# Performance work log

Hardware: AMD Instinct MI355X
Metric: run time of the kernel (lower is better)

The kernel has to match this reference:

```python
import jax, jax.numpy as jnp
import numpy as np

NV, NU, FT, HID, OUT, NE = 50000, 50000, 128, 256, 128, 800000


def _seg_sum(x, seg, n):
    return jax.ops.segment_sum(x, seg, num_segments=n)


def _seg_mean(x, seg, n):
    s = _seg_sum(x, seg, n)
    cnt = _seg_sum(jnp.ones((x.shape[0], 1), x.dtype), seg, n)
    return s / jnp.maximum(cnt, 1.0)


def _prelu(x, a):
    return jnp.where(x >= 0, x, a * x)


def setup_inputs() -> dict:
    key = jax.random.key(0)
    ks = jax.random.split(key, 12)
    lin = lambda k, i, o: jax.random.normal(k, (i, o), jnp.float32) * (1.0 / np.sqrt(i))
    slope = jnp.full((1,), 0.25, jnp.float32)  # nn.PReLU() default
    return {
        'features_v': jax.random.normal(ks[0], (NV, FT), jnp.float32),
        'features_u': jax.random.normal(ks[1], (NU, FT), jnp.float32),
        'edge_v': jax.random.randint(ks[2], (NE,), 0, NV, jnp.int32),
        'edge_u': jax.random.randint(ks[3], (NE,), 0, NU, jnp.int32),
        'Wv1': lin(ks[4], FT, HID), 'bv1': jnp.zeros((HID,), jnp.float32), 'av1': slope,
        'Wu1': lin(ks[5], FT, HID), 'bu1': jnp.zeros((HID,), jnp.float32), 'au1': slope,
        'Wv2': lin(ks[6], HID, OUT), 'bv2': jnp.zeros((OUT,), jnp.float32), 'av2': slope,
        'Wu2': lin(ks[7], HID, OUT), 'bu2': jnp.zeros((OUT,), jnp.float32), 'au2': slope,
        'Wv3': lin(ks[8], OUT + FT, OUT), 'bv3': jnp.zeros((OUT,), jnp.float32),
        'Wu3': lin(ks[9], OUT + FT, OUT), 'bu3': jnp.zeros((OUT,), jnp.float32),
    }


def reference(features_v, features_u, edge_v, edge_u,
              Wv1, bv1, av1, Wu1, bu1, au1,
              Wv2, bv2, av2, Wu2, bu2, au2,
              Wv3, bv3, Wu3, bu3):
    # stage 1: mean of raw neighbor features across the bipartite relation
    vneighbor = _seg_mean(features_u[edge_u], edge_v, NV)   # [NV, FT]
    uneighbor = _seg_mean(features_v[edge_v], edge_u, NU)   # [NU, FT]
    ve1 = _prelu(vneighbor @ Wv1 + bv1, av1)                # [NV, HID]
    ue1 = _prelu(uneighbor @ Wu1 + bu1, au1)                # [NU, HID]
    # stage 2: mean of transformed neighbor embeddings
    ve2 = _prelu(_seg_mean(ue1[edge_u], edge_v, NV) @ Wv2 + bv2, av2)  # [NV, OUT]
    ue2 = _prelu(_seg_mean(ve1[edge_v], edge_u, NU) @ Wu2 + bu2, au2)  # [NU, OUT]
    # stage 3: concat with raw features, Identity activation
    ve3 = jnp.concatenate([ve2, features_v], 1) @ Wv3 + bv3  # [NV, OUT]
    ue3 = jnp.concatenate([ue2, features_u], 1) @ Wu3 + bu3  # [NU, OUT]
    # self-inclusive neighbor mean: mean over {neighbors' emb, own emb}
    deg_v = _seg_sum(jnp.ones((NE, 1), ve3.dtype), edge_v, NV)
    deg_u = _seg_sum(jnp.ones((NE, 1), ue3.dtype), edge_u, NU)
    sv = (_seg_sum(ue3[edge_u], edge_v, NV) + ve3) / (deg_v + 1.0)  # [NV, OUT]
    su = (_seg_sum(ve3[edge_v], edge_u, NU) + ue3) / (deg_u + 1.0)  # [NU, OUT]
    # node_embs = mean over the single relation = (ve2, ue2); pack all outputs
    out_v = jnp.concatenate([ve2, sv], 1)  # [NV, 2*OUT]
    out_u = jnp.concatenate([ue2, su], 1)  # [NU, 2*OUT]
    return jnp.stack([out_v, out_u])       # [2, N, 2*OUT]
```

## Files before the change

### kernel.cpp

```cpp
#include <hip/hip_runtime.h>
#include <stdint.h>

#define NVN 50000
#define NUN 50000
#define NB 49
#define CH 4096
#define HCH 8192
#define BCAP 24576

typedef __attribute__((ext_vector_type(8))) short short8v;
typedef __attribute__((ext_vector_type(8))) unsigned short ushort8v;
typedef __attribute__((ext_vector_type(4))) float float4v;

__device__ __forceinline__ unsigned short f2bf(float f) {
  union { float f; unsigned u; } x; x.f = f;
  unsigned r = x.u + 0x7FFFu + ((x.u >> 16) & 1u);
  return (unsigned short)(r >> 16);
}
__device__ __forceinline__ float bf2f(unsigned short h) {
  union { unsigned u; float f; } x; x.u = ((unsigned)h) << 16;
  return x.f;
}

struct WConvEnt { const float* src; unsigned short* dst; int K; int N; };
struct PrepArgs {
  WConvEnt w[6];
  const float* fv; const float* fu;
  unsigned short* fbv; unsigned short* fbu;
  const int* ev; const int* eu;
  int* bcnt;
  int ne;
};
__global__ __launch_bounds__(256) void prep_kernel(PrepArgs a) {
  __shared__ int h[2 * NB];
  int b = blockIdx.x;
  if (b < 768) {
    WConvEnt c = a.w[b >> 7];
    int i = (b & 127) * 256 + threadIdx.x;
    int k = i / c.N, n = i - k * c.N;
    c.dst[(size_t)n * c.K + k] = f2bf(c.src[i]);
    return;
  }
  b -= 768;
  if (b < 6250) {
    const float* src = (b < 3125) ? a.fv : a.fu;
    unsigned short* dst = (b < 3125) ? a.fbv : a.fbu;
    int bb = (b < 3125) ? b : b - 3125;
    size_t base = ((size_t)bb * 256 + threadIdx.x) * 8;
    float4 x = *(const float4*)(src + base);
    float4 y = *(const float4*)(src + base + 4);
    ushort8v r;
    r[0] = f2bf(x.x); r[1] = f2bf(x.y); r[2] = f2bf(x.z); r[3] = f2bf(x.w);
    r[4] = f2bf(y.x); r[5] = f2bf(y.y); r[6] = f2bf(y.z); r[7] = f2bf(y.w);
    *(ushort8v*)(dst + base) = r;
    return;
  }
  b -= 6250;
  const int tid = threadIdx.x;
  for (int j = tid; j < 2 * NB; j += 256) h[j] = 0;
  __syncthreads();
  const int e0 = b * HCH;
  const int e1 = min(e0 + HCH, a.ne);
  for (int i = e0 + tid; i < e1; i += 256) {
    atomicAdd(&h[a.ev[i] >> 10], 1);
    atomicAdd(&h[NB + (a.eu[i] >> 10)], 1);
  }
  __syncthreads();
  for (int j = tid; j < 2 * NB; j += 256)
    if (h[j]) atomicAdd(&a.bcnt[j], h[j]);
}

__global__ __launch_bounds__(64) void tiny_scan(const int* __restrict__ bcnt,
                                                int* __restrict__ bbase,
                                                int* __restrict__ bcur) {
  if (threadIdx.x == 0) {
    int acc = 0;
    for (int b = 0; b < NB; ++b) { bbase[b] = acc; bcur[b] = acc; acc += bcnt[b]; }
    bbase[NB] = acc;
    acc = 0;
    for (int b = 0; b < NB; ++b) {
      bbase[NB + 1 + b] = acc; bcur[NB + b] = acc; acc += bcnt[NB + b];
    }
    bbase[2 * NB + 1] = acc;
  }
}

__global__ __launch_bounds__(256) void bucket_scatter(
    const int* __restrict__ ev, const int* __restrict__ eu,
    int* __restrict__ bcur_v, int* __restrict__ bcur_u,
    unsigned* __restrict__ stg_v, unsigned* __restrict__ stg_u, int ne) {
  __shared__ int cnt[NB];
  __shared__ int pos[NB];
  __shared__ int gbase[NB];
  __shared__ unsigned rec[CH];
  const int side = blockIdx.y;
  const int* key = side ? eu : ev;
  const int* pay = side ? ev : eu;
  int* bcur = side ? bcur_u : bcur_v;
  unsigned* stg = side ? stg_u : stg_v;
  const int tid = threadIdx.x;
  const int e0 = blockIdx.x * CH;
  const int e1 = min(e0 + CH, ne);
  if (tid < NB) cnt[tid] = 0;
  __syncthreads();
  for (int i = e0 + tid; i < e1; i += 256) atomicAdd(&cnt[key[i] >> 10], 1);
  __syncthreads();
  if (tid < 64) {
    int c = (tid < NB) ? cnt[tid] : 0;
    int x = c;
#pragma unroll
    for (int s = 1; s < 64; s <<= 1) {
      int t = __shfl_up(x, (unsigned)s, 64);
      if (tid >= s) x += t;
    }
    if (tid < NB) pos[tid] = x - c;
  }
  __syncthreads();
  for (int i = e0 + tid; i < e1; i += 256) {
    int k = key[i];
    int b = k >> 10;
    int p = atomicAdd(&pos[b], 1);
    rec[p] = ((unsigned)(k & 1023) << 16) | (unsigned)pay[i];
  }
  __syncthreads();
  if (tid < NB) gbase[tid] = atomicAdd(&bcur[tid], cnt[tid]);
  __syncthreads();
  for (int b = 0; b < NB; ++b) {
    int c = cnt[b];
    int lbase = pos[b] - c;
    int gb = gbase[b];
    for (int i = tid; i < c; i += 256) stg[gb + i] = rec[lbase + i];
  }
}

__global__ __launch_bounds__(256) void bucket_build(
    int* __restrict__ off_v, int* __restrict__ off_u,
    const int* __restrict__ bbase,
    const unsigned* __restrict__ stg_v, const unsigned* __restrict__ stg_u,
    unsigned short* __restrict__ csr_v, unsigned short* __restrict__ csr_u,
    int nv, int nu) {
  __shared__ int cur[1024];
  __shared__ int wred[4];
  __shared__ int wbase[4];
  __shared__ unsigned short st[BCAP];
  const int side = blockIdx.y;
  int* off = side ? off_u : off_v;
  const unsigned* stg = side ? stg_u : stg_v;
  unsigned short* csr = side ? csr_u : csr_v;
  const int n = side ? nu : nv;
  const int* bb = bbase + side * (NB + 1);
  const int nbase = blockIdx.x << 10;
  const int nb = min(1024, n - nbase);
  const int ebase = bb[blockIdx.x];
  const int cnt = bb[blockIdx.x + 1] - ebase;
  const int tid = threadIdx.x;
  const int lane = tid & 63;
  const int w = tid >> 6;

  for (int j = tid; j < 1024; j += 256) cur[j] = 0;
  __syncthreads();
  for (int i = tid; i < cnt; i += 256) atomicAdd(&cur[stg[ebase + i] >> 16], 1);
  __syncthreads();
  const int j0 = tid * 4;
  int c0 = cur[j0], c1 = cur[j0 + 1], c2 = cur[j0 + 2], c3 = cur[j0 + 3];
  int tsum = c0 + c1 + c2 + c3;
  int x = tsum;
#pragma unroll
  for (int s = 1; s < 64; s <<= 1) {
    int t = __shfl_up(x, (unsigned)s, 64);
    if (lane >= s) x += t;
  }
  if (lane == 63) wred[w] = x;
  __syncthreads();
  if (tid == 0) {
    int a = 0;
    for (int k = 0; k < 4; ++k) { wbase[k] = a; a += wred[k]; }
  }
  __syncthreads();
  const int ex = wbase[w] + (x - tsum);
  cur[j0] = ex;
  cur[j0 + 1] = ex + c0;
  cur[j0 + 2] = ex + c0 + c1;
  cur[j0 + 3] = ex + c0 + c1 + c2;
  __syncthreads();
  for (int j = tid; j < nb; j += 256) off[nbase + j] = ebase + cur[j];
  if (nbase + nb == n && tid == 0) off[n] = ebase + cnt;
  __syncthreads();
  if (cnt <= BCAP) {
    for (int i = tid; i < cnt; i += 256) {
      unsigned r = stg[ebase + i];
      int p = atomicAdd(&cur[r >> 16], 1);
      st[p] = (unsigned short)(r & 0xFFFFu);
    }
    __syncthreads();
    for (int i = tid; i < cnt; i += 256) csr[ebase + i] = st[i];
  } else {
    for (int i = tid; i < cnt; i += 256) {
      unsigned r = stg[ebase + i];
      int p = atomicAdd(&cur[r >> 16], 1);
      csr[ebase + p] = (unsigned short)(r & 0xFFFFu);
    }
  }
}

struct GSide {
  const unsigned* src;
  const unsigned short* csr; const int* off;
  const float* bias; const float* slope;
  const unsigned* own;
  void* dst; int ldo;
};

__device__ __forceinline__ void acc8(float* acc, uint4 p) {
  acc[0] += bf2f((unsigned short)p.x);
  acc[1] += bf2f((unsigned short)(p.x >> 16));
  acc[2] += bf2f((unsigned short)p.y);
  acc[3] += bf2f((unsigned short)(p.y >> 16));
  acc[4] += bf2f((unsigned short)p.z);
  acc[5] += bf2f((unsigned short)(p.z >> 16));
  acc[6] += bf2f((unsigned short)p.w);
  acc[7] += bf2f((unsigned short)(p.w >> 16));
}

template <int MODE>
__global__ __launch_bounds__(256) void gatherk(GSide g0, GSide g1, int n) {
  GSide g = blockIdx.y ? g1 : g0;
  int wid = (int)(((size_t)blockIdx.x * 256 + threadIdx.x) >> 6);
  if (wid >= n) return;
  const int lane = threadIdx.x & 63;
  const int grp = lane >> 4;
  const int lc = lane & 15;
  const int s = g.off[wid], e = g.off[wid + 1];
  const int cnt = e - s;
  float acc[8] = {0.f, 0.f, 0.f, 0.f, 0.f, 0.f, 0.f, 0.f};
  int idx = 0;
  if (lane < cnt) idx = (int)g.csr[s + lane];
  const int m = cnt < 64 ? cnt : 64;
  int j = 0;
  for (; j + 7 < m; j += 8) {
    int r0 = __shfl(idx, j + grp, 64);
    int r1 = __shfl(idx, j + 4 + grp, 64);
    uint4 p0 = *((const uint4*)(g.src + (size_t)r0 * 64) + lc);
    uint4 p1 = *((const uint4*)(g.src + (size_t)r1 * 64) + lc);
    acc8(acc, p0);
    acc8(acc, p1);
  }
  for (; j + 3 < m; j += 4) {
    int r0 = __shfl(idx, j + grp, 64);
    uint4 p0 = *((const uint4*)(g.src + (size_t)r0 * 64) + lc);
    acc8(acc, p0);
  }
  if (j < m) {
    int jj = j + grp;
    int r0 = __shfl(idx, jj < m ? jj : 0, 64);
    if (jj < m) {
      uint4 p0 = *((const uint4*)(g.src + (size_t)r0 * 64) + lc);
      acc8(acc, p0);
    }
  }
  for (int i = s + 64 + grp; i < e; i += 4) {
    int r0 = (int)g.csr[i];
    uint4 p0 = *((const uint4*)(g.src + (size_t)r0 * 64) + lc);
    acc8(acc, p0);
  }
#pragma unroll
  for (int k = 0; k < 8; ++k) {
    acc[k] += __shfl_xor(acc[k], 16, 64);
    acc[k] += __shfl_xor(acc[k], 32, 64);
  }
  if (grp != 0) return;
  const float deg = (float)cnt;
  if (MODE == 0) {
    float inv = 1.f / fmaxf(deg, 1.f);
    uint4 o;
    o.x = ((unsigned)f2bf(acc[1] * inv) << 16) | (unsigned)f2bf(acc[0] * inv);
    o.y = ((unsigned)f2bf(acc[3] * inv) << 16) | (unsigned)f2bf(acc[2] * inv);
    o.z = ((unsigned)f2bf(acc[5] * inv) << 16) | (unsigned)f2bf(acc[4] * inv);
    o.w = ((unsigned)f2bf(acc[7] * inv) << 16) | (unsigned)f2bf(acc[6] * inv);
    *((uint4*)((unsigned*)g.dst + (size_t)wid * g.ldo) + lc) = o;
  } else if (MODE == 1) {
    float inv = 1.f / fmaxf(deg, 1.f);
    float sl = g.slope[0];
    float4 b0 = *(const float4*)(g.bias + lc * 8);
    float4 b1 = *(const float4*)(g.bias + lc * 8 + 4);
    float o[8];
    o[0] = acc[0] * inv + b0.x; o[1] = acc[1] * inv + b0.y;
    o[2] = acc[2] * inv + b0.z; o[3] = acc[3] * inv + b0.w;
    o[4] = acc[4] * inv + b1.x; o[5] = acc[5] * inv + b1.y;
    o[6] = acc[6] * inv + b1.z; o[7] = acc[7] * inv + b1.w;
#pragma unroll
    for (int k = 0; k < 8; ++k) o[k] = o[k] >= 0.f ? o[k] : o[k] * sl;
    float* dp = (float*)g.dst + (size_t)wid * g.ldo + lc * 8;
    *(float4*)dp = make_float4(o[0], o[1], o[2], o[3]);
    *(float4*)(dp + 4) = make_float4(o[4], o[5], o[6], o[7]);
  } else {
    float inv = 1.f / (deg + 1.f);
    uint4 ow = *((const uint4*)(g.own + (size_t)wid * 64) + lc);
    float o[8];
    o[0] = (acc[0] + bf2f((unsigned short)ow.x)) * inv;
    o[1] = (acc[1] + bf2f((unsigned short)(ow.x >> 16))) * inv;
    o[2] = (acc[2] + bf2f((unsigned short)ow.y)) * inv;
    o[3] = (acc[3] + bf2f((unsigned short)(ow.y >> 16))) * inv;
    o[4] = (acc[4] + bf2f((unsigned short)ow.z)) * inv;
    o[5] = (acc[5] + bf2f((unsigned short)(ow.z >> 16))) * inv;
    o[6] = (acc[6] + bf2f((unsigned short)ow.w)) * inv;
    o[7] = (acc[7] + bf2f((unsigned short)(ow.w >> 16))) * inv;
    float* dp = (float*)g.dst + (size_t)wid * g.ldo + lc * 8;
    *(float4*)dp = make_float4(o[0], o[1], o[2], o[3]);
    *(float4*)(dp + 4) = make_float4(o[4], o[5], o[6], o[7]);
  }
}

struct GmSide {
  const void* A1; const void* A2;
  const unsigned short* Wt;
  const float* bias; const float* slope;
  void* C;
};

template <int BF>
__device__ __forceinline__ short8v load_a8(const void* A, size_t off) {
  if (BF) {
    return *(const short8v*)((const unsigned short*)A + off);
  } else {
    const float* p = (const float*)A + off;
    float4 x = *(const float4*)p;
    float4 y = *(const float4*)(p + 4);
    short8v r;
    r[0] = (short)f2bf(x.x); r[1] = (short)f2bf(x.y);
    r[2] = (short)f2bf(x.z); r[3] = (short)f2bf(x.w);
    r[4] = (short)f2bf(y.x); r[5] = (short)f2bf(y.y);
    r[6] = (short)f2bf(y.z); r[7] = (short)f2bf(y.w);
    return r;
  }
}

#define TILES 5

template <int KB1, int KB2, int NF, int A1BF, int A2BF, int CBF, int ACT>
__global__ __launch_bounds__(256) void gemm_reg(GmSide s0, GmSide s1,
                                                int lda1, int lda2,
                                                int ldc, int M) {
  constexpr int KB = KB1 + KB2;
  GmSide s = blockIdx.z ? s1 : s0;
  const int K = KB * 32;
  const int tid = threadIdx.x;
  const int wv = tid >> 6;
  const int lane = tid & 63;
  const int lc = lane & 15;
  const int khi = lane >> 4;
  const int bm = blockIdx.x * (16 * TILES);
  const int colbase = wv * (NF * 16);

  short8v b[KB][NF];
#pragma unroll
  for (int kb = 0; kb < KB; ++kb)
#pragma unroll
    for (int f = 0; f < NF; ++f)
      b[kb][f] = *(const short8v*)(s.Wt + (size_t)(colbase + f * 16 + lc) * K +
                                   kb * 32 + khi * 8);

  const float sl = ACT ? s.slope[0] : 0.f;
  float bias_f[NF];
#pragma unroll
  for (int f = 0; f < NF; ++f)
    bias_f[f] = s.bias ? s.bias[colbase + f * 16 + lc] : 0.f;

  short8v a_cur[KB], a_nxt[KB];
  {
    const int rowa = bm + lc;
#pragma unroll
    for (int kb = 0; kb < KB; ++kb) {
      if (kb < KB1)
        a_cur[kb] = load_a8<A1BF>(s.A1, (size_t)rowa * lda1 + kb * 32 + khi * 8);
      else
        a_cur[kb] = load_a8<A2BF>(s.A2, (size_t)rowa * lda2 + (kb - KB1) * 32 + khi * 8);
    }
  }

  for (int t = 0; t < TILES; ++t) {
    if (t + 1 < TILES) {
      const int rowa = bm + (t + 1) * 16 + lc;
#pragma unroll
      for (int kb = 0; kb < KB; ++kb) {
        if (kb < KB1)
          a_nxt[kb] = load_a8<A1BF>(s.A1, (size_t)rowa * lda1 + kb * 32 + khi * 8);
        else
          a_nxt[kb] = load_a8<A2BF>(s.A2, (size_t)rowa * lda2 + (kb - KB1) * 32 + khi * 8);
      }
    }
    float4v acc[NF];
#pragma unroll
    for (int f = 0; f < NF; ++f) acc[f] = (float4v){0.f, 0.f, 0.f, 0.f};
#pragma unroll
    for (int kb = 0; kb < KB; ++kb)
#pragma unroll
      for (int f = 0; f < NF; ++f)
        acc[f] = __builtin_amdgcn_mfma_f32_16x16x32_bf16(a_cur[kb], b[kb][f],
                                                         acc[f], 0, 0, 0);
#pragma unroll
    for (int f = 0; f < NF; ++f) {
      const int col = colbase + f * 16 + lc;
#pragma unroll
      for (int i = 0; i < 4; ++i) {
        const int row = bm + t * 16 + khi * 4 + i;
        float v = acc[f][i] + bias_f[f];
        if (ACT && v < 0.f) v *= sl;
        if (CBF) ((unsigned short*)s.C)[(size_t)row * ldc + col] = f2bf(v);
        else     ((float*)s.C)[(size_t)row * ldc + col] = v;
      }
    }
#pragma unroll
    for (int kb = 0; kb < KB; ++kb) a_cur[kb] = a_nxt[kb];
  }
}

extern "C" void kernel_launch(void* const* d_in, const int* in_sizes, int n_in,
                              void* d_out, int out_size, void* d_ws, size_t ws_size,
                              hipStream_t stream) {
  const float* features_v = (const float*)d_in[0];
  const float* features_u = (const float*)d_in[1];
  const int* edge_v = (const int*)d_in[2];
  const int* edge_u = (const int*)d_in[3];
  const float* Wv1 = (const float*)d_in[4];
  const float* bv1 = (const float*)d_in[5];
  const float* av1 = (const float*)d_in[6];
  const float* Wu1 = (const float*)d_in[7];
  const float* bu1 = (const float*)d_in[8];
  const float* au1 = (const float*)d_in[9];
  const float* Wv2 = (const float*)d_in[10];
  const float* bv2 = (const float*)d_in[11];
  const float* av2 = (const float*)d_in[12];
  const float* Wu2 = (const float*)d_in[13];
  const float* bu2 = (const float*)d_in[14];
  const float* au2 = (const float*)d_in[15];
  const float* Wv3 = (const float*)d_in[16];
  const float* bv3 = (const float*)d_in[17];
  const float* Wu3 = (const float*)d_in[18];
  const float* bu3 = (const float*)d_in[19];
  const int ne = in_sizes[2];

  int* bcnt = (int*)d_ws;
  int* bbase = bcnt + 2 * NB;
  int* bcur = bbase + 2 * (NB + 1);
  int* off_v = bcur + 2 * NB;
  int* off_u = off_v + NVN + 1;
  unsigned short* csr_v = (unsigned short*)(off_u + NUN + 1);
  unsigned short* csr_u = csr_v + ne;
  uintptr_t sbase = (((uintptr_t)(csr_u + ne)) + 15) & ~(uintptr_t)15;
  unsigned* stg_v = (unsigned*)sbase;
  unsigned* stg_u = stg_v + ne;
  unsigned short* P1b = (unsigned short*)(stg_u + ne);
  unsigned short* P2b = P1b + (size_t)NVN * 128;
  unsigned short* E1v = P2b + (size_t)NUN * 128;
  unsigned short* E1u = E1v + (size_t)NVN * 256;
  unsigned short* Wb = E1u + (size_t)NUN * 256;
  unsigned short* Fbv = Wb + 6 * 32768;
  unsigned short* Fbu = Fbv + (size_t)NVN * 128;
  unsigned short* Ve3b = E1v;
  unsigned short* Ue3b = E1u;

  float* out_v = (float*)d_out;
  float* out_u = out_v + (size_t)NVN * 256;

  const int hb = (ne + HCH - 1) / HCH;
  const dim3 gg((NVN * 64) / 256, 2);
  const dim3 gr(NVN / (16 * TILES), 1, 2);
  const dim3 gsc((ne + CH - 1) / CH, 2);
  const dim3 gbd(NB, 2);

  hipMemsetAsync(bcnt, 0, (size_t)(2 * NB) * 4, stream);
  PrepArgs pa;
  pa.w[0] = {Wv1, Wb + 0 * 32768, 128, 256};
  pa.w[1] = {Wu1, Wb + 1 * 32768, 128, 256};
  pa.w[2] = {Wv2, Wb + 2 * 32768, 256, 128};
  pa.w[3] = {Wu2, Wb + 3 * 32768, 256, 128};
  pa.w[4] = {Wv3, Wb + 4 * 32768, 256, 128};
  pa.w[5] = {Wu3, Wb + 5 * 32768, 256, 128};
  pa.fv = features_v; pa.fu = features_u;
  pa.fbv = Fbv; pa.fbu = Fbu;
  pa.ev = edge_v; pa.eu = edge_u;
  pa.bcnt = bcnt; pa.ne = ne;
  prep_kernel<<<768 + 6250 + hb, 256, 0, stream>>>(pa);
  tiny_scan<<<1, 64, 0, stream>>>(bcnt, bbase, bcur);
  bucket_scatter<<<gsc, 256, 0, stream>>>(edge_v, edge_u, bcur, bcur + NB,
                                          stg_v, stg_u, ne);
  bucket_build<<<gbd, 256, 0, stream>>>(off_v, off_u, bbase, stg_v, stg_u,
                                        csr_v, csr_u, NVN, NUN);

  {
    GSide a{(const unsigned*)Fbu, csr_v, off_v, nullptr, nullptr, nullptr, P1b, 64};
    GSide b{(const unsigned*)Fbv, csr_u, off_u, nullptr, nullptr, nullptr, P2b, 64};
    gatherk<0><<<gg, 256, 0, stream>>>(a, b, NVN);
  }
  {
    GmSide a{P1b, nullptr, Wb + 0 * 32768, bv1, av1, E1v};
    GmSide b{P2b, nullptr, Wb + 1 * 32768, bu1, au1, E1u};
    gemm_reg<4, 0, 4, 1, 0, 1, 1><<<gr, 256, 0, stream>>>(a, b, 128, 0, 256, NVN);
  }
  {
    GmSide a{E1v, nullptr, Wb + 3 * 32768, nullptr, nullptr, P1b};
    GmSide b{E1u, nullptr, Wb + 2 * 32768, nullptr, nullptr, P2b};
    gemm_reg<8, 0, 2, 1, 0, 1, 0><<<gr, 256, 0, stream>>>(a, b, 256, 0, 128, NVN);
  }
  {
    GSide a{(const unsigned*)P2b, csr_v, off_v, bv2, av2, nullptr, out_v, 256};
    GSide b{(const unsigned*)P1b, csr_u, off_u, bu2, au2, nullptr, out_u, 256};
    gatherk<1><<<gg, 256, 0, stream>>>(a, b, NVN);
  }
  {
    GmSide a{out_v, Fbv, Wb + 4 * 32768, bv3, nullptr, Ve3b};
    GmSide b{out_u, Fbu, Wb + 5 * 32768, bu3, nullptr, Ue3b};
    gemm_reg<4, 4, 2, 0, 1, 1, 0><<<gr, 256, 0, stream>>>(a, b, 256, 128, 128, NVN);
  }
  {
    GSide a{(const unsigned*)Ue3b, csr_v, off_v, nullptr, nullptr,
            (const unsigned*)Ve3b, out_v + 128, 256};
    GSide b{(const unsigned*)Ve3b, csr_u, off_u, nullptr, nullptr,
            (const unsigned*)Ue3b, out_u + 128, 256};
    gatherk<2><<<gg, 256, 0, stream>>>(a, b, NVN);
  }
}
```

Measured before the change: 422.8 us.

## Fuse layer-1 and layer-2 GEMMs via LDS and fold bucket scan into consumers

Replaces the two back-to-back GEMMs (P→E1 with bias+PReLU, then E1→P·W2) with a single kernel that keeps the 64x256 E1 tile in shared memory, so the 256-wide bf16 intermediate is never written to or re-read from global memory. The tiny single-thread scan kernel is removed: bucket_scatter and bucket_build each recompute the 49-bucket prefix sum with a wave shuffle, and bcur becomes a relative cursor zeroed by memset. This saves a launch and a large intermediate round trip. In exchange the fused kernel holds many register fragments and a 33KB LDS tile, which may reduce occupancy. It also writes its output in place over P1b/P2b, which is safe only because each block reads its own rows into registers before writing them back.

```diff
diff --git a/kernel.cpp b/kernel.cpp
--- a/kernel.cpp
+++ b/kernel.cpp
@@ -70,39 +70,35 @@
     if (h[j]) atomicAdd(&a.bcnt[j], h[j]);
 }
 
-__global__ __launch_bounds__(64) void tiny_scan(const int* __restrict__ bcnt,
-                                                int* __restrict__ bbase,
-                                                int* __restrict__ bcur) {
-  if (threadIdx.x == 0) {
-    int acc = 0;
-    for (int b = 0; b < NB; ++b) { bbase[b] = acc; bcur[b] = acc; acc += bcnt[b]; }
-    bbase[NB] = acc;
-    acc = 0;
-    for (int b = 0; b < NB; ++b) {
-      bbase[NB + 1 + b] = acc; bcur[NB + b] = acc; acc += bcnt[NB + b];
-    }
-    bbase[2 * NB + 1] = acc;
-  }
-}
-
 __global__ __launch_bounds__(256) void bucket_scatter(
     const int* __restrict__ ev, const int* __restrict__ eu,
-    int* __restrict__ bcur_v, int* __restrict__ bcur_u,
+    const int* __restrict__ bcnt, int* __restrict__ bcur,
     unsigned* __restrict__ stg_v, unsigned* __restrict__ stg_u, int ne) {
   __shared__ int cnt[NB];
   __shared__ int pos[NB];
   __shared__ int gbase[NB];
+  __shared__ int bb_s[NB];
   __shared__ unsigned rec[CH];
   const int side = blockIdx.y;
   const int* key = side ? eu : ev;
   const int* pay = side ? ev : eu;
-  int* bcur = side ? bcur_u : bcur_v;
   unsigned* stg = side ? stg_u : stg_v;
   const int tid = threadIdx.x;
   const int e0 = blockIdx.x * CH;
   const int e1 = min(e0 + CH, ne);
   if (tid < NB) cnt[tid] = 0;
   __syncthreads();
+  if (tid >= 64 && tid < 128) {
+    int t = tid - 64;
+    int c = (t < NB) ? bcnt[side * NB + t] : 0;
+    int x = c;
+#pragma unroll
+    for (int s = 1; s < 64; s <<= 1) {
+      int tt = __shfl_up(x, (unsigned)s, 64);
+      if (t >= s) x += tt;
+    }
+    if (t < NB) bb_s[t] = x - c;
+  }
   for (int i = e0 + tid; i < e1; i += 256) atomicAdd(&cnt[key[i] >> 10], 1);
   __syncthreads();
   if (tid < 64) {
@@ -123,7 +119,8 @@
     rec[p] = ((unsigned)(k & 1023) << 16) | (unsigned)pay[i];
   }
   __syncthreads();
-  if (tid < NB) gbase[tid] = atomicAdd(&bcur[tid], cnt[tid]);
+  if (tid < NB)
+    gbase[tid] = bb_s[tid] + atomicAdd(&bcur[side * NB + tid], cnt[tid]);
   __syncthreads();
   for (int b = 0; b < NB; ++b) {
     int c = cnt[b];
@@ -135,30 +132,39 @@
 
 __global__ __launch_bounds__(256) void bucket_build(
     int* __restrict__ off_v, int* __restrict__ off_u,
-    const int* __restrict__ bbase,
+    const int* __restrict__ bcnt,
     const unsigned* __restrict__ stg_v, const unsigned* __restrict__ stg_u,
     unsigned short* __restrict__ csr_v, unsigned short* __restrict__ csr_u,
     int nv, int nu) {
   __shared__ int cur[1024];
   __shared__ int wred[4];
   __shared__ int wbase[4];
+  __shared__ int bb_s[NB + 1];
   __shared__ unsigned short st[BCAP];
   const int side = blockIdx.y;
   int* off = side ? off_u : off_v;
   const unsigned* stg = side ? stg_u : stg_v;
   unsigned short* csr = side ? csr_u : csr_v;
   const int n = side ? nu : nv;
-  const int* bb = bbase + side * (NB + 1);
-  const int nbase = blockIdx.x << 10;
-  const int nb = min(1024, n - nbase);
-  const int ebase = bb[blockIdx.x];
-  const int cnt = bb[blockIdx.x + 1] - ebase;
   const int tid = threadIdx.x;
   const int lane = tid & 63;
   const int w = tid >> 6;
-
+  if (tid < 64) {
+    int c = (tid < NB) ? bcnt[side * NB + tid] : 0;
+    int x = c;
+#pragma unroll
+    for (int s = 1; s < 64; s <<= 1) {
+      int t = __shfl_up(x, (unsigned)s, 64);
+      if (tid >= s) x += t;
+    }
+    if (tid <= NB) bb_s[tid] = x - c;
+  }
   for (int j = tid; j < 1024; j += 256) cur[j] = 0;
   __syncthreads();
+  const int nbase = blockIdx.x << 10;
+  const int nb = min(1024, n - nbase);
+  const int ebase = bb_s[blockIdx.x];
+  const int cnt = bb_s[blockIdx.x + 1] - ebase;
   for (int i = tid; i < cnt; i += 256) atomicAdd(&cur[stg[ebase + i] >> 16], 1);
   __syncthreads();
   const int j0 = tid * 4;
@@ -308,6 +314,110 @@
     float* dp = (float*)g.dst + (size_t)wid * g.ldo + lc * 8;
     *(float4*)dp = make_float4(o[0], o[1], o[2], o[3]);
     *(float4*)(dp + 4) = make_float4(o[4], o[5], o[6], o[7]);
+  }
+}
+
+struct Gm12Side {
+  const unsigned short* A;
+  const unsigned short* Wt1;
+  const float* bias1; const float* slope1;
+  const unsigned short* Wt2;
+  unsigned short* T;
+};
+
+__global__ __launch_bounds__(256) void gemm12(Gm12Side s0, Gm12Side s1, int M) {
+  __shared__ unsigned short e1[64][264];
+  const Gm12Side s = blockIdx.z ? s1 : s0;
+  const int tid = threadIdx.x;
+  const int wv = tid >> 6;
+  const int lane = tid & 63;
+  const int lc = lane & 15;
+  const int khi = lane >> 4;
+  const int bm = blockIdx.x * 64;
+
+  short8v b1[4][4];
+#pragma unroll
+  for (int kb = 0; kb < 4; ++kb)
+#pragma unroll
+    for (int f = 0; f < 4; ++f)
+      b1[kb][f] = *(const short8v*)(s.Wt1 + (size_t)(wv * 64 + f * 16 + lc) * 128 +
+                                    kb * 32 + khi * 8);
+  short8v a[4][4];
+#pragma unroll
+  for (int rt = 0; rt < 4; ++rt) {
+    const int row = bm + rt * 16 + lc;
+#pragma unroll
+    for (int kb = 0; kb < 4; ++kb) {
+      if (row < M)
+        a[rt][kb] = *(const short8v*)(s.A + (size_t)row * 128 + kb * 32 + khi * 8);
+      else
+        a[rt][kb] = (short8v){0, 0, 0, 0, 0, 0, 0, 0};
+    }
+  }
+  float4v acc[4][4];
+#pragma unroll
+  for (int rt = 0; rt < 4; ++rt)
+#pragma unroll
+    for (int f = 0; f < 4; ++f) acc[rt][f] = (float4v){0.f, 0.f, 0.f, 0.f};
+#pragma unroll
+  for (int kb = 0; kb < 4; ++kb)
+#pragma unroll
+    for (int rt = 0; rt < 4; ++rt)
+#pragma unroll
+      for (int f = 0; f < 4; ++f)
+        acc[rt][f] = __builtin_amdgcn_mfma_f32_16x16x32_bf16(a[rt][kb], b1[kb][f],
+                                                             acc[rt][f], 0, 0, 0);
+  const float sl = s.slope1[0];
+#pragma unroll
+  for (int f = 0; f < 4; ++f) {
+    const int col = wv * 64 + f * 16 + lc;
+    const float bv = s.bias1[col];
+#pragma unroll
+    for (int rt = 0; rt < 4; ++rt)
+#pragma unroll
+      for (int i = 0; i < 4; ++i) {
+        float v = acc[rt][f][i] + bv;
+        if (v < 0.f) v *= sl;
+        e1[rt * 16 + khi * 4 + i][col] = f2bf(v);
+      }
+  }
+  __syncthreads();
+
+  short8v b2[8][2];
+#pragma unroll
+  for (int kb = 0; kb < 8; ++kb)
+#pragma unroll
+    for (int f = 0; f < 2; ++f)
+      b2[kb][f] = *(const short8v*)(s.Wt2 + (size_t)(wv * 32 + f * 16 + lc) * 256 +
+                                    kb * 32 + khi * 8);
+  float4v acc2[4][2];
+#pragma unroll
+  for (int rt = 0; rt < 4; ++rt)
+#pragma unroll
+    for (int f = 0; f < 2; ++f) acc2[rt][f] = (float4v){0.f, 0.f, 0.f, 0.f};
+#pragma unroll
+  for (int kb = 0; kb < 8; ++kb) {
+    short8v a2[4];
+#pragma unroll
+    for (int rt = 0; rt < 4; ++rt)
+      a2[rt] = *(const short8v*)(&e1[rt * 16 + lc][kb * 32 + khi * 8]);
+#pragma unroll
+    for (int rt = 0; rt < 4; ++rt)
+#pragma unroll
+      for (int f = 0; f < 2; ++f)
+        acc2[rt][f] = __builtin_amdgcn_mfma_f32_16x16x32_bf16(a2[rt], b2[kb][f],
+                                                              acc2[rt][f], 0, 0, 0);
+  }
+#pragma unroll
+  for (int f = 0; f < 2; ++f) {
+    const int col = wv * 32 + f * 16 + lc;
+#pragma unroll
+    for (int rt = 0; rt < 4; ++rt)
+#pragma unroll
+      for (int i = 0; i < 4; ++i) {
+        const int row = bm + rt * 16 + khi * 4 + i;
+        if (row < M) s.T[(size_t)row * 128 + col] = f2bf(acc2[rt][f][i]);
+      }
   }
 }
 
@@ -441,8 +551,7 @@
   const int ne = in_sizes[2];
 
   int* bcnt = (int*)d_ws;
-  int* bbase = bcnt + 2 * NB;
-  int* bcur = bbase + 2 * (NB + 1);
+  int* bcur = bcnt + 2 * NB;
   int* off_v = bcur + 2 * NB;
   int* off_u = off_v + NVN + 1;
   unsigned short* csr_v = (unsigned short*)(off_u + NUN + 1);
@@ -452,13 +561,11 @@
   unsigned* stg_u = stg_v + ne;
   unsigned short* P1b = (unsigned short*)(stg_u + ne);
   unsigned short* P2b = P1b + (size_t)NVN * 128;
-  unsigned short* E1v = P2b + (size_t)NUN * 128;
-  unsigned short* E1u = E1v + (size_t)NVN * 256;
-  unsigned short* Wb = E1u + (size_t)NUN * 256;
+  unsigned short* Ve3b = P2b + (size_t)NUN * 128;
+  unsigned short* Ue3b = Ve3b + (size_t)NVN * 128;
+  unsigned short* Wb = Ue3b + (size_t)NUN * 128;
   unsigned short* Fbv = Wb + 6 * 32768;
   unsigned short* Fbu = Fbv + (size_t)NVN * 128;
-  unsigned short* Ve3b = E1v;
-  unsigned short* Ue3b = E1u;
 
   float* out_v = (float*)d_out;
   float* out_u = out_v + (size_t)NVN * 256;
@@ -466,10 +573,11 @@
   const int hb = (ne + HCH - 1) / HCH;
   const dim3 gg((NVN * 64) / 256, 2);
   const dim3 gr(NVN / (16 * TILES), 1, 2);
+  const dim3 g12((NVN + 63) / 64, 1, 2);
   const dim3 gsc((ne + CH - 1) / CH, 2);
   const dim3 gbd(NB, 2);
 
-  hipMemsetAsync(bcnt, 0, (size_t)(2 * NB) * 4, stream);
+  hipMemsetAsync(bcnt, 0, (size_t)(4 * NB) * 4, stream);
   PrepArgs pa;
   pa.w[0] = {Wv1, Wb + 0 * 32768, 128, 256};
   pa.w[1] = {Wu1, Wb + 1 * 32768, 128, 256};
@@ -482,10 +590,9 @@
   pa.ev = edge_v; pa.eu = edge_u;
   pa.bcnt = bcnt; pa.ne = ne;
   prep_kernel<<<768 + 6250 + hb, 256, 0, stream>>>(pa);
-  tiny_scan<<<1, 64, 0, stream>>>(bcnt, bbase, bcur);
-  bucket_scatter<<<gsc, 256, 0, stream>>>(edge_v, edge_u, bcur, bcur + NB,
+  bucket_scatter<<<gsc, 256, 0, stream>>>(edge_v, edge_u, bcnt, bcur,
                                           stg_v, stg_u, ne);
-  bucket_build<<<gbd, 256, 0, stream>>>(off_v, off_u, bbase, stg_v, stg_u,
+  bucket_build<<<gbd, 256, 0, stream>>>(off_v, off_u, bcnt, stg_v, stg_u,
                                         csr_v, csr_u, NVN, NUN);
 
   {
@@ -494,14 +601,9 @@
     gatherk<0><<<gg, 256, 0, stream>>>(a, b, NVN);
   }
   {
-    GmSide a{P1b, nullptr, Wb + 0 * 32768, bv1, av1, E1v};
-    GmSide b{P2b, nullptr, Wb + 1 * 32768, bu1, au1, E1u};
-    gemm_reg<4, 0, 4, 1, 0, 1, 1><<<gr, 256, 0, stream>>>(a, b, 128, 0, 256, NVN);
-  }
-  {
-    GmSide a{E1v, nullptr, Wb + 3 * 32768, nullptr, nullptr, P1b};
-    GmSide b{E1u, nullptr, Wb + 2 * 32768, nullptr, nullptr, P2b};
-    gemm_reg<8, 0, 2, 1, 0, 1, 0><<<gr, 256, 0, stream>>>(a, b, 256, 0, 128, NVN);
+    Gm12Side a{P1b, Wb + 0 * 32768, bv1, av1, Wb + 3 * 32768, P1b};
+    Gm12Side b{P2b, Wb + 1 * 32768, bu1, au1, Wb + 2 * 32768, P2b};
+    gemm12<<<g12, 256, 0, stream>>>(a, b, NVN);
   }
   {
     GSide a{(const unsigned*)P2b, csr_v, off_v, bv2, av2, nullptr, out_v, 256};
```

After: 392.9 us. -7.1%, faster.
